# Performance work log

Hardware: AMD Instinct MI355X
Metric: run time of the kernel (lower is better)

## Reference

```python
import jax, jax.numpy as jnp
import numpy as np

BLOCK = 8
MAN = 7  # bf16-style mantissa bits


def _ste(x, qx):
    # straight-through estimator: forward = qx, backward = identity
    return x + jax.lax.stop_gradient(qx - x)


def bf16_q(x):
    # fake-quantize to bfloat16 (exp=8, man=7, round-to-nearest)
    return _ste(x, x.astype(jnp.bfloat16).astype(x.dtype))


def bfp_q(x, axis):
    # block floating point: shared exponent per block of 8 along `axis`,
    # 7 mantissa bits relative to floor(log2(max|block|)).
    xm = jnp.moveaxis(x, axis, -1)
    shp = xm.shape
    xb = xm.reshape(shp[:-1] + (shp[-1] // BLOCK, BLOCK))
    maxabs = jnp.max(jnp.abs(xb), axis=-1, keepdims=True)
    _, e = jnp.frexp(maxabs)              # maxabs = m * 2^e, m in [0.5, 1)
    step = jnp.exp2((e - 1 - MAN).astype(x.dtype))  # 2^(floor(log2(maxabs)) - MAN)
    q = jnp.round(xb / step) * step
    q = jnp.where(maxabs > 0, q, jnp.zeros_like(q))
    q = jnp.moveaxis(q.reshape(shp), -1, axis)
    return _ste(x, q)


def _lstm(layer_input, h0, c0, U, V, bih, bhh):
    HS = h0.shape[-1]
    # weight/bias quantization is step-invariant -> hoist out of the scan
    Ut_q = bfp_q(U.T, axis=0)   # [input_size, 4*HS], blocks along dim0
    Vt_q = bfp_q(V.T, axis=0)   # [HS, 4*HS]
    b_q = bf16_q(bih) + bf16_q(bhh)

    def step(carry, x_t):
        h, c = carry
        x_q = bfp_q(x_t, axis=1)          # [B, input_size]
        h_q = bfp_q(h, axis=1)            # [B, HS]
        gates = bf16_q(x_q @ Ut_q + h_q @ Vt_q + b_q)  # [B, 4*HS]
        i_t, f_t, g_t, o_t = jnp.split(gates, 4, axis=1)
        i_t = bf16_q(jax.nn.sigmoid(i_t))
        f_t = bf16_q(jax.nn.sigmoid(f_t))
        g_t = bf16_q(jnp.tanh(g_t))
        o_t = bf16_q(jax.nn.sigmoid(o_t))
        c = bf16_q(f_t * c + i_t * g_t)
        h = bf16_q(o_t * jnp.tanh(c))
        return (h, c), h

    (h_T, c_T), out = jax.lax.scan(step, (h0, c0), layer_input)
    return out, h_T, c_T


def setup_inputs() -> dict:
    key = jax.random.key(0)
    ks = jax.random.split(key, 7)
    S, B, D, HS = 512, 64, 1024, 1024
    return {
        "layer_input": jax.random.normal(ks[0], (S, B, D), jnp.float32),
        "h_t": jax.random.normal(ks[1], (B, HS), jnp.float32),
        "c_t": jax.random.normal(ks[2], (B, HS), jnp.float32),
        "U": jax.random.normal(ks[3], (4 * HS, D), jnp.float32) / np.sqrt(D),
        "V": jax.random.normal(ks[4], (4 * HS, HS), jnp.float32) / np.sqrt(HS),
        "bih": jax.random.normal(ks[5], (4 * HS,), jnp.float32) * 0.1,
        "bhh": jax.random.normal(ks[6], (4 * HS,), jnp.float32) * 0.1,
    }


def reference(layer_input, h_t, c_t, U, V, bih, bhh):
    out, h_T, c_T = _lstm(layer_input, h_t, c_t, U, V, bih, bhh)
    return out, (h_T, c_T)
```

## Files before the change

kernel.cpp:

```cpp
#include <hip/hip_runtime.h>
#include <stdint.h>

typedef __attribute__((ext_vector_type(4))) float f32x4;
typedef __attribute__((ext_vector_type(8))) short bf16x8;
typedef __attribute__((ext_vector_type(4))) int i32x4;
typedef unsigned short ushort_t;
typedef unsigned long long u64;

#define S_LEN 512
#define BATCH 64
#define HSZ   1024
#define G4    4096
#define NWG   256
#define NTHR  256
#define SMEM_BYTES (65536 + 65536 + 32 * 33 * 4)


__device__ __forceinline__ float bf16r(float x) {
    union { float f; uint32_t u; } v; v.f = x;
    v.u = (v.u + 0x7FFFu + ((v.u >> 16) & 1u)) & 0xFFFF0000u;
    return v.f;
}

__device__ __forceinline__ ushort_t bf16bits(float x) {
    union { float f; uint32_t u; } v; v.f = x;
    uint32_t r = v.u + 0x7FFFu + ((v.u >> 16) & 1u);
    return (ushort_t)(r >> 16);
}

__device__ __forceinline__ void bfp8_quant(const float v[8], ushort_t o[8]) {
    float m = 0.f;
    #pragma unroll
    for (int i = 0; i < 8; ++i) m = fmaxf(m, fabsf(v[i]));
    if (m > 0.f) {
        int e;
        (void)frexpf(m, &e);
        float inv_step = ldexpf(1.0f, 8 - e);
        float step     = ldexpf(1.0f, e - 8);
        #pragma unroll
        for (int i = 0; i < 8; ++i) {
            float q = rintf(v[i] * inv_step) * step;
            o[i] = bf16bits(q);
        }
    } else {
        #pragma unroll
        for (int i = 0; i < 8; ++i) o[i] = 0;
    }
}

__device__ __forceinline__ void bfp8_store(const float* __restrict__ src,
                                           ushort_t* __restrict__ dst) {
    float v[8];
    float4 a = ((const float4*)src)[0];
    float4 b = ((const float4*)src)[1];
    v[0]=a.x; v[1]=a.y; v[2]=a.z; v[3]=a.w;
    v[4]=b.x; v[5]=b.y; v[6]=b.z; v[7]=b.w;
    union { ushort_t us[8]; int4 i4; } o;
    bfp8_quant(v, o.us);
    *(int4*)dst = o.i4;
}

__device__ __forceinline__ ushort_t bfp_one(float v, float m) {
    if (!(m > 0.f)) return 0;
    int e;
    (void)frexpf(m, &e);
    float q = rintf(ldexpf(v, 8 - e)) * ldexpf(1.f, e - 8);
    return bf16bits(q);
}


__global__ __launch_bounds__(256) void quant_weights_pack(
    const float* __restrict__ U, const float* __restrict__ V,
    ushort_t* __restrict__ Up, ushort_t* __restrict__ Vp,
    const float* __restrict__ bih, const float* __restrict__ bhh,
    float* __restrict__ bq)
{
    int blk = blockIdx.x * 256 + threadIdx.x;
    int mtx = blk >> 19;
    int r = blk & 524287;
    int n = r >> 7, kb = r & 127;
    int q = n >> 10, j = n & 1023;
    int gslice = j >> 3, jj = j & 7;
    int cc = q * 8 + jj;
    const float* src = (mtx == 0 ? U : V) + (size_t)n * 1024 + kb * 8;
    ushort_t* dst = (mtx == 0 ? Up : Vp) + ((size_t)gslice * 32 + cc) * 1024 + kb * 8;
    bfp8_store(src, dst);
    if (blk < 4096) bq[blk] = bf16r(bih[blk]) + bf16r(bhh[blk]);
}

__global__ __launch_bounds__(256) void init_state(
    const float* __restrict__ h0, const float* __restrict__ c0,
    ushort_t* __restrict__ hq0, float* __restrict__ c_ws)
{
    int idx = blockIdx.x * 256 + threadIdx.x;
    int b = idx >> 7, j0 = (idx & 127) * 8;
    bfp8_store(h0 + (size_t)b * 1024 + j0, hq0 + (size_t)b * 1024 + j0);
    const float4* src = (const float4*)(c0 + (size_t)b * 1024 + j0);
    float4* dst = (float4*)(c_ws + (size_t)b * 1024 + j0);
    dst[0] = src[0]; dst[1] = src[1];
}

__global__ __launch_bounds__(256) void quant_x_all(
    const float* __restrict__ x, ushort_t* __restrict__ xq)
{
    int idx = blockIdx.x * 256 + threadIdx.x;
    int r = idx >> 7, j0 = (idx & 127) * 8;
    bfp8_store(x + (size_t)r * 1024 + j0, xq + (size_t)r * 1024 + j0);
}


__device__ __forceinline__ f32x4 mm32_frag(const bf16x8 a[32],
                                           const char* __restrict__ bbase,
                                           int bswz, int lg16, f32x4 acc) {
    f32x4 acc2 = {0.f, 0.f, 0.f, 0.f};
    #pragma unroll
    for (int i = 0; i < 32; i += 2) {
        bf16x8 b0 = *(const bf16x8*)(bbase + ((i * 64 + lg16) ^ bswz));
        bf16x8 b1 = *(const bf16x8*)(bbase + (((i + 1) * 64 + lg16) ^ bswz));
        acc  = __builtin_amdgcn_mfma_f32_16x16x32_bf16(a[i],     b0, acc,  0, 0, 0);
        acc2 = __builtin_amdgcn_mfma_f32_16x16x32_bf16(a[i + 1], b1, acc2, 0, 0, 0);
    }
    return acc + acc2;
}

__device__ __forceinline__ f32x4 mm32_hv(const ushort_t* __restrict__ hrow,
                                         const char* __restrict__ Blds,
                                         int brow, int lg16, f32x4 acc) {
    union { i32x4 i; bf16x8 v; } a[32];
    #pragma unroll
    for (int i = 0; i < 32; ++i) {
        asm volatile("global_load_dwordx4 %0, %1, off sc1"
                     : "=v"(a[i].i)
                     : "v"(hrow + i * 32));
    }
    asm volatile("s_waitcnt vmcnt(0)" ::: "memory");
    __builtin_amdgcn_sched_barrier(0);
    bf16x8 af[32];
    #pragma unroll
    for (int i = 0; i < 32; ++i) af[i] = a[i].v;
    return mm32_frag(af, Blds + brow * 2048, (brow & 15) << 4, lg16, acc);
}

__device__ __forceinline__ f32x4 mm32_xq(const ushort_t* __restrict__ xrow,
                                         const char* __restrict__ Blds,
                                         int brow, int lg16, f32x4 acc) {
    bf16x8 a[32];
    #pragma unroll
    for (int i = 0; i < 32; ++i)
        a[i] = *(const bf16x8*)(xrow + i * 32);
    return mm32_frag(a, Blds + brow * 2048, (brow & 15) << 4, lg16, acc);
}

__device__ __forceinline__ f32x4 mm32_xu(const float* __restrict__ xrow,
                                         const char* __restrict__ Blds,
                                         int brow, int lg16, f32x4 acc) {
    const int bswz = (brow & 15) << 4;
    const char* bbase = Blds + brow * 2048;
    f32x4 acc2 = {0.f, 0.f, 0.f, 0.f};
    #pragma unroll
    for (int c = 0; c < 4; ++c) {
        float4 f[8][2];
        #pragma unroll
        for (int i = 0; i < 8; ++i) {
            f[i][0] = *(const float4*)(xrow + (c * 8 + i) * 32);
            f[i][1] = *(const float4*)(xrow + (c * 8 + i) * 32 + 4);
        }
        #pragma unroll
        for (int i = 0; i < 8; ++i) {
            float vv[8] = { f[i][0].x, f[i][0].y, f[i][0].z, f[i][0].w,
                            f[i][1].x, f[i][1].y, f[i][1].z, f[i][1].w };
            union { ushort_t us[8]; bf16x8 v; } aa;
            bfp8_quant(vv, aa.us);
            int kb = c * 8 + i;
            bf16x8 b = *(const bf16x8*)(bbase + ((kb * 64 + lg16) ^ bswz));
            if (kb & 1) acc2 = __builtin_amdgcn_mfma_f32_16x16x32_bf16(aa.v, b, acc2, 0, 0, 0);
            else        acc  = __builtin_amdgcn_mfma_f32_16x16x32_bf16(aa.v, b, acc,  0, 0, 0);
        }
    }
    return acc + acc2;
}


__global__ __launch_bounds__(256, 1) void lstm_persist(
    const float* __restrict__ x,
    const ushort_t* __restrict__ xq,
    const ushort_t* __restrict__ Up,
    const ushort_t* __restrict__ Vp,
    const float* __restrict__ bq,
    const float* __restrict__ c0_ws,
    ushort_t* __restrict__ hq0, ushort_t* __restrict__ hq1,
    float* __restrict__ out, float* __restrict__ hT, float* __restrict__ cT,
    unsigned int* __restrict__ barrier_cnt)
{
    extern __shared__ char smem[];
    char* Vlds = smem;
    char* Ulds = smem + 65536;
    float* gbuf = (float*)(smem + 131072);

    const int tid = threadIdx.x;
    const int bx = blockIdx.x;
    const int gs = bx & 127;
    const int ms = bx >> 7;
    const int j0 = gs * 8;
    const int lane = tid & 63, wid = tid >> 6;
    const int wm = wid >> 1, wn = wid & 1;
    const int lr = lane & 15, lg = lane >> 4;
    const int lg16 = lg * 16;
    const int brow = wn * 16 + lr;
    const int arow = ms * 32 + wm * 16 + lr;
    const bool use_xq = (xq != nullptr);

    {
        const int4* upg = (const int4*)(Up + (size_t)gs * 32 * 1024);
        const int4* vpg = (const int4*)(Vp + (size_t)gs * 32 * 1024);
        for (int idx = tid; idx < 4096; idx += NTHR) {
            int row = idx >> 7, kc = idx & 127;
            int off = row * 2048 + ((kc * 16) ^ ((row & 15) << 4));
            *(int4*)(Ulds + off) = upg[idx];
            *(int4*)(Vlds + off) = vpg[idx];
        }
    }
    __syncthreads();

    const int q_gate = brow >> 3;
    const float bqv = bq[q_gate * 1024 + j0 + (brow & 7)];
    const f32x4 bq4 = {bqv, bqv, bqv, bqv};

    const int urow = tid >> 3, ujj = tid & 7;
    const int bg = ms * 32 + urow;
    float c_reg = c0_ws[(size_t)bg * 1024 + j0 + ujj];

    unsigned int* cnt = barrier_cnt + ms * 256;
    unsigned int* myc = cnt + (bx & 7) * 32;

    f32x4 xUacc = use_xq
        ? mm32_xq(xq + (size_t)arow * 1024 + lg * 8, Ulds, brow, lg16, bq4)
        : mm32_xu(x  + (size_t)arow * 1024 + lg * 8, Ulds, brow, lg16, bq4);

    for (int t = 0; t < S_LEN; ++t) {
        const bool doX = (t < S_LEN - 1);
        const ushort_t* hin = (t & 1) ? hq1 : hq0;
        ushort_t* hout = ((t + 1) & 1) ? hq1 : hq0;

        f32x4 accG = mm32_hv(hin + (size_t)arow * 1024 + lg * 8, Vlds, brow, lg16, xUacc);

        #pragma unroll
        for (int r = 0; r < 4; ++r) {
            float gate = bf16r(accG[r]);
            float sig = 1.f / (1.f + expf(-gate));
            float th  = tanhf(gate);
            float act = bf16r(q_gate == 2 ? th : sig);
            gbuf[(wm * 16 + lg * 4 + r) * 33 + brow] = act;
        }
        __syncthreads();

        float i_t = gbuf[urow * 33 + ujj];
        float f_t = gbuf[urow * 33 + 8 + ujj];
        float g_t = gbuf[urow * 33 + 16 + ujj];
        float o_t = gbuf[urow * 33 + 24 + ujj];
        float cn = bf16r(__fadd_rn(__fmul_rn(f_t, c_reg), __fmul_rn(i_t, g_t)));
        float hn = bf16r(__fmul_rn(o_t, tanhf(cn)));
        c_reg = cn;

        {
            float m = fabsf(hn);
            m = fmaxf(m, __shfl_xor(m, 1));
            m = fmaxf(m, __shfl_xor(m, 2));
            m = fmaxf(m, __shfl_xor(m, 4));
            uint32_t hv = (uint32_t)bfp_one(hn, m);
            uint32_t p1 = __shfl_xor(hv, 1);
            uint32_t w32 = hv | (p1 << 16);
            uint32_t p2 = __shfl_xor(w32, 2);
            u64 w64 = ((u64)p2 << 32) | (u64)w32;
            if ((ujj & 3) == 0) {
                u64* dst = (u64*)(hout + (size_t)bg * 1024 + j0) + (ujj >> 2);
                __hip_atomic_store(dst, w64, __ATOMIC_RELAXED, __HIP_MEMORY_SCOPE_AGENT);
            }
        }

        if (doX) {
            __syncthreads();
            if (tid == 0)
                __hip_atomic_fetch_add(myc, 1u, __ATOMIC_RELAXED, __HIP_MEMORY_SCOPE_AGENT);
        }

        __builtin_nontemporal_store(hn, out + (size_t)t * (BATCH * HSZ) + (size_t)bg * 1024 + j0 + ujj);
        if (t == S_LEN - 1) {
            __builtin_nontemporal_store(hn, hT + (size_t)bg * 1024 + j0 + ujj);
            __builtin_nontemporal_store(cn, cT + (size_t)bg * 1024 + j0 + ujj);
        }

        if (doX) {
            f32x4 accX = use_xq
                ? mm32_xq(xq + (size_t)(t + 1) * (BATCH * HSZ) + (size_t)arow * 1024 + lg * 8,
                          Ulds, brow, lg16, bq4)
                : mm32_xu(x  + (size_t)(t + 1) * (BATCH * HSZ) + (size_t)arow * 1024 + lg * 8,
                          Ulds, brow, lg16, bq4);

            if (wid == 0) {
                const unsigned tgt = 128u * (unsigned)(t + 1);
                while (true) {
                    unsigned v = (lane < 8)
                        ? __hip_atomic_load(cnt + lane * 32, __ATOMIC_RELAXED, __HIP_MEMORY_SCOPE_AGENT)
                        : 0u;
                    #pragma unroll
                    for (int s = 1; s < 64; s <<= 1)
                        v += (unsigned)__shfl_xor((int)v, s);
                    if (v >= tgt) break;
                    __builtin_amdgcn_s_sleep(1);
                }
            }
            __syncthreads();
            xUacc = accX;
        }
    }
}


extern "C" void kernel_launch(void* const* d_in, const int* in_sizes, int n_in,
                              void* d_out, int out_size, void* d_ws, size_t ws_size,
                              hipStream_t stream) {
    const float* x   = (const float*)d_in[0];
    const float* h0  = (const float*)d_in[1];
    const float* c0  = (const float*)d_in[2];
    const float* U   = (const float*)d_in[3];
    const float* V   = (const float*)d_in[4];
    const float* bih = (const float*)d_in[5];
    const float* bhh = (const float*)d_in[6];

    float* out = (float*)d_out;
    float* hT  = out + (size_t)S_LEN * BATCH * HSZ;
    float* cT  = hT + (size_t)BATCH * HSZ;

    char* p = (char*)d_ws;
    ushort_t* Up  = (ushort_t*)p; p += (size_t)G4 * 1024 * 2;
    ushort_t* Vp  = (ushort_t*)p; p += (size_t)G4 * 1024 * 2;
    float* bq     = (float*)p;    p += (size_t)G4 * 4;
    float* c_ws   = (float*)p;    p += (size_t)BATCH * HSZ * 4;
    ushort_t* hq0 = (ushort_t*)p; p += (size_t)BATCH * HSZ * 2;
    ushort_t* hq1 = (ushort_t*)p; p += (size_t)BATCH * HSZ * 2;
    unsigned int* cnt = (unsigned int*)p; p += 2048;
    p = (char*)(((uintptr_t)p + 255) & ~(uintptr_t)255);
    size_t xq_bytes = (size_t)S_LEN * BATCH * HSZ * 2;
    ushort_t* xq = nullptr;
    if ((size_t)(p - (char*)d_ws) + xq_bytes <= ws_size)
        xq = (ushort_t*)p;

    hipMemsetAsync(cnt, 0, 2048, stream);
    hipLaunchKernelGGL(quant_weights_pack, dim3(4096), dim3(256), 0, stream,
                       U, V, Up, Vp, bih, bhh, bq);
    hipLaunchKernelGGL(init_state, dim3(32), dim3(256), 0, stream, h0, c0, hq0, c_ws);
    if (xq)
        hipLaunchKernelGGL(quant_x_all, dim3(16384), dim3(256), 0, stream, x, xq);

    hipFuncSetAttribute(reinterpret_cast<const void*>(lstm_persist),
                        hipFuncAttributeMaxDynamicSharedMemorySize, SMEM_BYTES);

    void* args[] = {
        (void*)&x, (void*)&xq, (void*)&Up, (void*)&Vp, (void*)&bq, (void*)&c_ws,
        (void*)&hq0, (void*)&hq1,
        (void*)&out, (void*)&hT, (void*)&cT, (void*)&cnt
    };
    hipLaunchCooperativeKernel(reinterpret_cast<void*>(lstm_persist),
                               dim3(NWG), dim3(NTHR), args, SMEM_BYTES, stream);
}
```

Measured before the change: 5.135 ms.

## Stage h tile in LDS cooperatively and stream U weights from global

Result: slower. 5.586 ms (+8.8%).

```diff
diff --git a/kernel.cpp b/kernel.cpp
--- a/kernel.cpp
+++ b/kernel.cpp
@@ -109,61 +109,60 @@
 }
 
 
-__device__ __forceinline__ f32x4 mm32_frag(const bf16x8 a[32],
-                                           const char* __restrict__ bbase,
-                                           int bswz, int lg16, f32x4 acc) {
+__device__ __forceinline__ f32x4 mm32_ll(const char* __restrict__ Alds, int arow,
+                                         const char* __restrict__ Blds, int brow,
+                                         int lg16, f32x4 acc) {
+    const int aswz = (arow & 15) << 4;
+    const int bswz = (brow & 15) << 4;
+    const char* abase = Alds + arow * 2048;
+    const char* bbase = Blds + brow * 2048;
     f32x4 acc2 = {0.f, 0.f, 0.f, 0.f};
     #pragma unroll
     for (int i = 0; i < 32; i += 2) {
+        bf16x8 a0 = *(const bf16x8*)(abase + ((i * 64 + lg16) ^ aswz));
         bf16x8 b0 = *(const bf16x8*)(bbase + ((i * 64 + lg16) ^ bswz));
+        bf16x8 a1 = *(const bf16x8*)(abase + (((i + 1) * 64 + lg16) ^ aswz));
         bf16x8 b1 = *(const bf16x8*)(bbase + (((i + 1) * 64 + lg16) ^ bswz));
-        acc  = __builtin_amdgcn_mfma_f32_16x16x32_bf16(a[i],     b0, acc,  0, 0, 0);
-        acc2 = __builtin_amdgcn_mfma_f32_16x16x32_bf16(a[i + 1], b1, acc2, 0, 0, 0);
+        acc  = __builtin_amdgcn_mfma_f32_16x16x32_bf16(a0, b0, acc,  0, 0, 0);
+        acc2 = __builtin_amdgcn_mfma_f32_16x16x32_bf16(a1, b1, acc2, 0, 0, 0);
     }
     return acc + acc2;
 }
 
-__device__ __forceinline__ f32x4 mm32_hv(const ushort_t* __restrict__ hrow,
-                                         const char* __restrict__ Blds,
-                                         int brow, int lg16, f32x4 acc) {
-    union { i32x4 i; bf16x8 v; } a[32];
+__device__ __forceinline__ f32x4 mm32_gg(const ushort_t* __restrict__ ap,
+                                         const ushort_t* __restrict__ bp,
+                                         f32x4 acc) {
+    f32x4 acc2 = {0.f, 0.f, 0.f, 0.f};
     #pragma unroll
-    for (int i = 0; i < 32; ++i) {
-        asm volatile("global_load_dwordx4 %0, %1, off sc1"
-                     : "=v"(a[i].i)
-                     : "v"(hrow + i * 32));
-    }
-    asm volatile("s_waitcnt vmcnt(0)" ::: "memory");
-    __builtin_amdgcn_sched_barrier(0);
-    bf16x8 af[32];
-    #pragma unroll
-    for (int i = 0; i < 32; ++i) af[i] = a[i].v;
-    return mm32_frag(af, Blds + brow * 2048, (brow & 15) << 4, lg16, acc);
-}
-
-__device__ __forceinline__ f32x4 mm32_xq(const ushort_t* __restrict__ xrow,
-                                         const char* __restrict__ Blds,
-                                         int brow, int lg16, f32x4 acc) {
-    bf16x8 a[32];
-    #pragma unroll
-    for (int i = 0; i < 32; ++i)
-        a[i] = *(const bf16x8*)(xrow + i * 32);
-    return mm32_frag(a, Blds + brow * 2048, (brow & 15) << 4, lg16, acc);
-}
-
-__device__ __forceinline__ f32x4 mm32_xu(const float* __restrict__ xrow,
-                                         const char* __restrict__ Blds,
-                                         int brow, int lg16, f32x4 acc) {
-    const int bswz = (brow & 15) << 4;
-    const char* bbase = Blds + brow * 2048;
+    for (int c = 0; c < 4; ++c) {
+        bf16x8 a[8], b[8];
+        #pragma unroll
+        for (int i = 0; i < 8; ++i) {
+            a[i] = *(const bf16x8*)(ap + (c * 8 + i) * 32);
+            b[i] = *(const bf16x8*)(bp + (c * 8 + i) * 32);
+        }
+        #pragma unroll
+        for (int i = 0; i < 8; ++i) {
+            if (i & 1) acc2 = __builtin_amdgcn_mfma_f32_16x16x32_bf16(a[i], b[i], acc2, 0, 0, 0);
+            else       acc  = __builtin_amdgcn_mfma_f32_16x16x32_bf16(a[i], b[i], acc,  0, 0, 0);
+        }
+    }
+    return acc + acc2;
+}
+
+__device__ __forceinline__ f32x4 mm32_xu_g(const float* __restrict__ xrow,
+                                           const ushort_t* __restrict__ bp,
+                                           f32x4 acc) {
     f32x4 acc2 = {0.f, 0.f, 0.f, 0.f};
     #pragma unroll
     for (int c = 0; c < 4; ++c) {
         float4 f[8][2];
+        bf16x8 b[8];
         #pragma unroll
         for (int i = 0; i < 8; ++i) {
             f[i][0] = *(const float4*)(xrow + (c * 8 + i) * 32);
             f[i][1] = *(const float4*)(xrow + (c * 8 + i) * 32 + 4);
+            b[i] = *(const bf16x8*)(bp + (c * 8 + i) * 32);
         }
         #pragma unroll
         for (int i = 0; i < 8; ++i) {
@@ -171,10 +170,8 @@
                             f[i][1].x, f[i][1].y, f[i][1].z, f[i][1].w };
             union { ushort_t us[8]; bf16x8 v; } aa;
             bfp8_quant(vv, aa.us);
-            int kb = c * 8 + i;
-            bf16x8 b = *(const bf16x8*)(bbase + ((kb * 64 + lg16) ^ bswz));
-            if (kb & 1) acc2 = __builtin_amdgcn_mfma_f32_16x16x32_bf16(aa.v, b, acc2, 0, 0, 0);
-            else        acc  = __builtin_amdgcn_mfma_f32_16x16x32_bf16(aa.v, b, acc,  0, 0, 0);
+            if (i & 1) acc2 = __builtin_amdgcn_mfma_f32_16x16x32_bf16(aa.v, b[i], acc2, 0, 0, 0);
+            else       acc  = __builtin_amdgcn_mfma_f32_16x16x32_bf16(aa.v, b[i], acc,  0, 0, 0);
         }
     }
     return acc + acc2;
@@ -194,7 +191,7 @@
 {
     extern __shared__ char smem[];
     char* Vlds = smem;
-    char* Ulds = smem + 65536;
+    char* Hlds = smem + 65536;
     float* gbuf = (float*)(smem + 131072);
 
     const int tid = threadIdx.x;
@@ -207,16 +204,17 @@
     const int lr = lane & 15, lg = lane >> 4;
     const int lg16 = lg * 16;
     const int brow = wn * 16 + lr;
-    const int arow = ms * 32 + wm * 16 + lr;
+    const int arow_l = wm * 16 + lr;
+    const int arow = ms * 32 + arow_l;
     const bool use_xq = (xq != nullptr);
 
     {
-        const int4* upg = (const int4*)(Up + (size_t)gs * 32 * 1024);
         const int4* vpg = (const int4*)(Vp + (size_t)gs * 32 * 1024);
-        for (int idx = tid; idx < 4096; idx += NTHR) {
+        #pragma unroll
+        for (int it = 0; it < 16; ++it) {
+            int idx = tid + it * 256;
             int row = idx >> 7, kc = idx & 127;
             int off = row * 2048 + ((kc * 16) ^ ((row & 15) << 4));
-            *(int4*)(Ulds + off) = upg[idx];
             *(int4*)(Vlds + off) = vpg[idx];
         }
     }
@@ -225,6 +223,7 @@
     const int q_gate = brow >> 3;
     const float bqv = bq[q_gate * 1024 + j0 + (brow & 7)];
     const f32x4 bq4 = {bqv, bqv, bqv, bqv};
+    const ushort_t* Ub = Up + ((size_t)gs * 32 + brow) * 1024 + lg * 8;
 
     const int urow = tid >> 3, ujj = tid & 7;
     const int bg = ms * 32 + urow;
@@ -234,15 +233,35 @@
     unsigned int* myc = cnt + (bx & 7) * 32;
 
     f32x4 xUacc = use_xq
-        ? mm32_xq(xq + (size_t)arow * 1024 + lg * 8, Ulds, brow, lg16, bq4)
-        : mm32_xu(x  + (size_t)arow * 1024 + lg * 8, Ulds, brow, lg16, bq4);
+        ? mm32_gg(xq + (size_t)arow * 1024 + lg * 8, Ub, bq4)
+        : mm32_xu_g(x + (size_t)arow * 1024 + lg * 8, Ub, bq4);
 
     for (int t = 0; t < S_LEN; ++t) {
         const bool doX = (t < S_LEN - 1);
         const ushort_t* hin = (t & 1) ? hq1 : hq0;
         ushort_t* hout = ((t + 1) & 1) ? hq1 : hq0;
 
-        f32x4 accG = mm32_hv(hin + (size_t)arow * 1024 + lg * 8, Vlds, brow, lg16, xUacc);
+        {
+            const ushort_t* hsrc = hin + (size_t)ms * 32 * 1024;
+            i32x4 hb[16];
+            #pragma unroll
+            for (int i = 0; i < 16; ++i) {
+                asm volatile("global_load_dwordx4 %0, %1, off sc1"
+                             : "=v"(hb[i])
+                             : "v"(hsrc + ((size_t)(tid + i * 256)) * 8));
+            }
+            asm volatile("s_waitcnt vmcnt(0)" ::: "memory");
+            __builtin_amdgcn_sched_barrier(0);
+            #pragma unroll
+            for (int i = 0; i < 16; ++i) {
+                int c = tid + i * 256;
+                int r = c >> 7, kb = (c & 127) * 16;
+                *(i32x4*)(Hlds + r * 2048 + (kb ^ ((r & 15) << 4))) = hb[i];
+            }
+        }
+        __syncthreads();
+
+        f32x4 accG = mm32_ll(Hlds, arow_l, Vlds, brow, lg16, xUacc);
 
         #pragma unroll
         for (int r = 0; r < 4; ++r) {
@@ -292,10 +311,8 @@
 
         if (doX) {
             f32x4 accX = use_xq
-                ? mm32_xq(xq + (size_t)(t + 1) * (BATCH * HSZ) + (size_t)arow * 1024 + lg * 8,
-                          Ulds, brow, lg16, bq4)
-                : mm32_xu(x  + (size_t)(t + 1) * (BATCH * HSZ) + (size_t)arow * 1024 + lg * 8,
-                          Ulds, brow, lg16, bq4);
+                ? mm32_gg(xq + (size_t)(t + 1) * (BATCH * HSZ) + (size_t)arow * 1024 + lg * 8, Ub, bq4)
+                : mm32_xu_g(x + (size_t)(t + 1) * (BATCH * HSZ) + (size_t)arow * 1024 + lg * 8, Ub, bq4);
 
             if (wid == 0) {
                 const unsigned tgt = 128u * (unsigned)(t + 1);
```
